# Kernel optimization log

Hardware: AMD Instinct MI355X
Metric: run time of the kernel (lower is better)

## Reference

```python
import jax, jax.numpy as jnp
import numpy as np

N, B, F, MAXDEG = 100000, 4096, 128, 128
NEI = [25, 10]          # FLAGS.num_neighbors = '25_10'
E1, E2 = 128, 64        # FLAGS.encoder = '128_64'
DEC, C = 256, 50        # FLAGS.decoder, num_classes


def setup_inputs() -> dict:
    key = jax.random.key(0)
    ks = jax.random.split(key, 12)
    return {
        'nodes': jax.random.randint(ks[0], (B,), 0, N),
        'adj_info': jax.random.randint(ks[1], (N, MAXDEG), 0, N),
        'degrees': jax.random.uniform(ks[2], (N,), minval=1.0, maxval=float(MAXDEG)),
        'features': jax.random.normal(ks[3], (N, F), dtype=jnp.float32),
        'W0': jax.random.normal(ks[4], (F, E1), dtype=jnp.float32) / np.sqrt(F),
        'Wm': jax.random.normal(ks[5], (E1, E2), dtype=jnp.float32) / np.sqrt(E1),
        'Ws': jax.random.normal(ks[6], (E1, E2), dtype=jnp.float32) / np.sqrt(E1),
        'W1': jax.random.normal(ks[7], (E2, DEC), dtype=jnp.float32) / np.sqrt(E2),
        'b1': jnp.zeros((DEC,), jnp.float32),
        'W2': jax.random.normal(ks[8], (DEC, C), dtype=jnp.float32) / np.sqrt(DEC),
        'b2': jnp.zeros((C,), jnp.float32),
    }


def _gc(self_v, neigh_v, neigh_d, W, act):
    # GraphSAGE-style degree-normalized mean aggregation + shared linear map
    neigh_mean = jnp.mean(neigh_v / neigh_d, axis=1)   # [n, d_in]
    return act((self_v + neigh_mean) @ W)


def reference(nodes, adj_info, degrees, features, W0, Wm, Ws, W1, b1, W2, b2):
    key = jax.random.key(42)
    k1, k2, k3 = jax.random.split(key, 3)
    # --- uniform neighbor sampling (shared column shuffle, as in TF code) ---
    # hop 1: t = L-1 -> NEI[1] = 10 samples per seed node
    p1 = jax.random.permutation(k1, MAXDEG)[: NEI[1]]
    nb1 = adj_info[nodes][:, p1].reshape(-1)            # [10*B]
    # hop 2: t = 0 -> NEI[0] = 25 samples per hop-1 node
    p2 = jax.random.permutation(k2, MAXDEG)[: NEI[0]]
    nb2 = adj_info[nb1][:, p2].reshape(-1)              # [250*B]

    samples = [nodes, nb1, nb2]
    deg = [degrees[s] for s in samples]
    x = [features[s] for s in samples]                  # [B,F],[10B,F],[250B,F]

    tanh = jnp.tanh
    # layer 0: convolve hops 0 and 1 with shared W0
    h0 = _gc(x[0], x[1].reshape(B, NEI[1], F), deg[1].reshape(B, NEI[1], 1), W0, tanh)
    h1 = _gc(x[1], x[2].reshape(NEI[1] * B, NEI[0], F), deg[2].reshape(NEI[1] * B, NEI[0], 1), W0, tanh)
    # layer 1 (last): mean / std heads, linear activation, hop 0 only
    ident = lambda t: t
    z_mean = _gc(h0, h1.reshape(B, NEI[1], E1), deg[1].reshape(B, NEI[1], 1), Wm, ident)
    z_std = _gc(h0, h1.reshape(B, NEI[1], E1), deg[1].reshape(B, NEI[1], 1), Ws, ident)
    # reparameterized sample (std head = log-std)
    eps = jax.random.normal(k3, z_mean.shape, dtype=z_mean.dtype)
    z = z_mean + eps * jnp.exp(z_std)
    # decoder MLP + softmax class prediction (S = 1 MC sample)
    logits = jax.nn.relu(z @ W1 + b1) @ W2 + b2
    return jax.nn.softmax(logits, axis=-1)
```

## Files before the change

kernel.cpp:

```cpp
#include <hip/hip_runtime.h>
#include <hip/hip_bf16.h>
#include <hip/hip_fp16.h>
#include <stdint.h>
#include <stddef.h>

#define NNODES  100000
#define BATCH   4096
#define FDIM    128
#define MAXDEG  128
#define NEI0    25
#define NEI1    10
#define E1D     128
#define E2D     64
#define DECD    256
#define NCLS    50

#define NH1     (BATCH * NEI1)
#define NROWS   (NH1 + BATCH)

typedef _Float16 half8 __attribute__((ext_vector_type(8)));
typedef float f32x4 __attribute__((ext_vector_type(4)));
typedef float f32x2 __attribute__((ext_vector_type(2)));

__host__ __device__ inline void tf2x32(uint32_t k0, uint32_t k1,
                                       uint32_t x0, uint32_t x1,
                                       uint32_t* o0, uint32_t* o1) {
  uint32_t ks[3] = {k0, k1, k0 ^ k1 ^ 0x1BD11BDAu};
  x0 += ks[0]; x1 += ks[1];
  const int rot[2][4] = {{13, 15, 26, 6}, {17, 29, 16, 24}};
  for (int i = 0; i < 5; ++i) {
    const int* r = rot[i & 1];
    for (int j = 0; j < 4; ++j) {
      x0 += x1;
      x1 = (x1 << r[j]) | (x1 >> (32 - r[j]));
      x1 ^= x0;
    }
    x0 += ks[(i + 1) % 3];
    x1 += ks[(i + 2) % 3] + (uint32_t)(i + 1);
  }
  *o0 = x0; *o1 = x1;
}

__device__ inline float erfinv_xla(float x) {
  float w = -log1pf(-x * x);
  float p;
  if (w < 5.0f) {
    w = w - 2.5f;
    p = 2.81022636e-08f;
    p = 3.43273939e-07f  + p * w;
    p = -3.5233877e-06f  + p * w;
    p = -4.39150654e-06f + p * w;
    p = 0.00021858087f   + p * w;
    p = -0.00125372503f  + p * w;
    p = -0.00417768164f  + p * w;
    p = 0.246640727f     + p * w;
    p = 1.50140941f      + p * w;
  } else {
    w = sqrtf(w) - 3.0f;
    p = -0.000200214257f;
    p = 0.000100950558f  + p * w;
    p = 0.00134934322f   + p * w;
    p = -0.00367342844f  + p * w;
    p = 0.00573950773f   + p * w;
    p = -0.0076224613f   + p * w;
    p = 0.00943887047f   + p * w;
    p = 1.00167406f      + p * w;
    p = 2.83297682f      + p * w;
  }
  return p * x;
}

struct PermArgs { int p1[NEI1]; int p2[NEI0]; };

#define CAST_FBLKS 12500
#define W0HT_BLKS  8
#define WMST_BLKS  8
#define W1T_BLKS   8
#define W2P_BLKS   8
#define NB1_BLKS   160

__global__ __launch_bounds__(256) void prep_kernel(const float* __restrict__ f,
                                                   uint8_t* __restrict__ fh8,
                                                   const float* __restrict__ W0,
                                                   __half* __restrict__ W0ht,
                                                   const float* __restrict__ Wm,
                                                   const float* __restrict__ Wsd,
                                                   __half* __restrict__ Wmst,
                                                   const float* __restrict__ W1,
                                                   __half* __restrict__ W1t,
                                                   const float* __restrict__ W2,
                                                   __half* __restrict__ W2p,
                                                   const int* __restrict__ nodes,
                                                   const int* __restrict__ adj,
                                                   const float* __restrict__ degrees,
                                                   int* __restrict__ nb1,
                                                   float* __restrict__ invd1, PermArgs pa) {
  int bx = blockIdx.x;
  if (bx < CAST_FBLKS) {
    int i = bx * 256 + threadIdx.x;
    float4 v = ((const float4*)f)[i];
    int p = 0;
    p = __builtin_amdgcn_cvt_pk_fp8_f32(v.x, v.y, p, false);
    p = __builtin_amdgcn_cvt_pk_fp8_f32(v.z, v.w, p, true);
    ((int*)fh8)[i] = p;
    return;
  }
  bx -= CAST_FBLKS;
  if (bx < W0HT_BLKS) {
    int i = bx * 256 + threadIdx.x;
    int n = i >> 4, kb = (i & 15) * 8;
    uint4 ov; uint32_t* op = (uint32_t*)&ov;
#pragma unroll
    for (int q = 0; q < 4; ++q) {
      __half2 h = __floats2half2_rn(W0[(size_t)(kb + 2 * q) * E1D + n],
                                    W0[(size_t)(kb + 2 * q + 1) * E1D + n]);
      op[q] = __builtin_bit_cast(uint32_t, h);
    }
    *(uint4*)(W0ht + (size_t)n * FDIM + kb) = ov;
    return;
  }
  bx -= W0HT_BLKS;
  if (bx < WMST_BLKS) {
    int i = bx * 256 + threadIdx.x;
    int n = i >> 4, kb = (i & 15) * 8;
    const float* src = (n < E2D) ? (Wm + n) : (Wsd + (n - E2D));
    uint4 ov; uint32_t* op = (uint32_t*)&ov;
#pragma unroll
    for (int q = 0; q < 4; ++q) {
      __half2 h = __floats2half2_rn(src[(size_t)(kb + 2 * q) * E2D],
                                    src[(size_t)(kb + 2 * q + 1) * E2D]);
      op[q] = __builtin_bit_cast(uint32_t, h);
    }
    *(uint4*)(Wmst + (size_t)n * E1D + kb) = ov;
    return;
  }
  bx -= WMST_BLKS;
  if (bx < W1T_BLKS) {
    int i = bx * 256 + threadIdx.x;
    int n = i >> 3, kb = (i & 7) * 8;
    uint4 ov; uint32_t* op = (uint32_t*)&ov;
#pragma unroll
    for (int q = 0; q < 4; ++q) {
      __half2 h = __floats2half2_rn(W1[(size_t)(kb + 2 * q) * DECD + n],
                                    W1[(size_t)(kb + 2 * q + 1) * DECD + n]);
      op[q] = __builtin_bit_cast(uint32_t, h);
    }
    *(uint4*)(W1t + (size_t)n * E2D + kb) = ov;
    return;
  }
  bx -= W1T_BLKS;
  if (bx < W2P_BLKS) {
    int i = bx * 256 + threadIdx.x;
    int c = i >> 5, kb = (i & 31) * 8;
    uint4 ov; uint32_t* op = (uint32_t*)&ov;
#pragma unroll
    for (int q = 0; q < 4; ++q) {
      float a = (c < NCLS) ? W2[(size_t)(kb + 2 * q) * NCLS + c] : 0.0f;
      float b = (c < NCLS) ? W2[(size_t)(kb + 2 * q + 1) * NCLS + c] : 0.0f;
      __half2 h = __floats2half2_rn(a, b);
      op[q] = __builtin_bit_cast(uint32_t, h);
    }
    *(uint4*)(W2p + (size_t)c * DECD + kb) = ov;
    return;
  }
  bx -= W2P_BLKS;
  {
    int i = bx * 256 + threadIdx.x;
    int b = i / NEI1, j = i - b * NEI1;
    int nn = adj[(size_t)nodes[b] * MAXDEG + pa.p1[j]];
    nb1[i] = nn;
    invd1[i] = 1.0f / degrees[nn];
  }
}

#define P2_BLKS   4000
#define SELF_BLKS 2816

__global__ __launch_bounds__(256) void prep2_kernel(const int* __restrict__ nodes,
                                                    const int* __restrict__ nb1,
                                                    const int* __restrict__ adj,
                                                    const float* __restrict__ degrees,
                                                    const float* __restrict__ features,
                                                    int* __restrict__ nb2,
                                                    float* __restrict__ invd2,
                                                    __half* __restrict__ selfh, PermArgs pa) {
  int bx = blockIdx.x;
  if (bx < P2_BLKS) {
    int i = bx * 256 + threadIdx.x;
    int r = i / NEI0, j = i - r * NEI0;
    int nn = adj[(size_t)nb1[r] * MAXDEG + pa.p2[j]];
    nb2[i] = nn;
    invd2[i] = 1.0f / degrees[nn];
    return;
  }
  {
    int i = (bx - P2_BLKS) * 256 + threadIdx.x;
    int row = i >> 4, cq = (i & 15) * 8;
    int nid = (row < NH1) ? nb1[row] : nodes[row - NH1];
    const float* src = features + (size_t)nid * FDIM + cq;
    float4 a = *(const float4*)src;
    float4 b = *(const float4*)(src + 4);
    uint4 ov; uint32_t* op = (uint32_t*)&ov;
    op[0] = __builtin_bit_cast(uint32_t, __floats2half2_rn(a.x, a.y));
    op[1] = __builtin_bit_cast(uint32_t, __floats2half2_rn(a.z, a.w));
    op[2] = __builtin_bit_cast(uint32_t, __floats2half2_rn(b.x, b.y));
    op[3] = __builtin_bit_cast(uint32_t, __floats2half2_rn(b.z, b.w));
    *(uint4*)(selfh + (size_t)row * FDIM + cq) = ov;
  }
}

#define CONSV8(vv, idv) do { \
    float id_ = (idv); \
    f32x2 c0_ = __builtin_amdgcn_cvt_pk_f32_fp8((int)(vv).x, false); \
    f32x2 c1_ = __builtin_amdgcn_cvt_pk_f32_fp8((int)(vv).x, true); \
    f32x2 c2_ = __builtin_amdgcn_cvt_pk_f32_fp8((int)(vv).y, false); \
    f32x2 c3_ = __builtin_amdgcn_cvt_pk_f32_fp8((int)(vv).y, true); \
    acc0 += c0_[0] * id_; acc1 += c0_[1] * id_; \
    acc2 += c1_[0] * id_; acc3 += c1_[1] * id_; \
    acc4 += c2_[0] * id_; acc5 += c2_[1] * id_; \
    acc6 += c3_[0] * id_; acc7 += c3_[1] * id_; \
  } while (0)

#define H8(x) __builtin_bit_cast(half8, x)

__global__ __launch_bounds__(256) void sage0_kernel(const int* __restrict__ nodes,
                                                    const int* __restrict__ nb1,
                                                    const float* __restrict__ invd1,
                                                    const int* __restrict__ nb2,
                                                    const float* __restrict__ invd2,
                                                    const uint8_t* __restrict__ fh8,
                                                    const __half* __restrict__ selfh,
                                                    const __half* __restrict__ W0ht,
                                                    __half* __restrict__ hh) {
  const int t = threadIdx.x;
  const int blk = blockIdx.x;
  const bool typeA = blk < (NH1 / 16);
  const int row_base = typeA ? blk * 16 : NH1 + (blk - NH1 / 16) * 16;
  __shared__ int    nn_lds[16][NEI0];
  __shared__ float  id_lds[16][NEI0];
  __shared__ __half agg_h[16][FDIM];

  if (typeA) {
    for (int i = t; i < 16 * NEI0; i += 256) {
      int r = i / NEI0, j = i - r * NEI0;
      nn_lds[r][j] = nb2[row_base * NEI0 + i];
      id_lds[r][j] = invd2[row_base * NEI0 + i];
    }
  } else {
    const int sb = row_base - NH1;
    if (t < 16 * NEI1) {
      int r = t / NEI1, j = t - r * NEI1;
      nn_lds[r][j] = nb1[sb * NEI1 + t];
      id_lds[r][j] = invd1[sb * NEI1 + t];
    }
  }
  __syncthreads();

  const int l = t & 63, w = t >> 6;
  const int r  = w * 4 + (l >> 4);
  const int c0 = (l & 15) * 8;
  const uint8_t* fr8 = fh8 + c0;
  const int*   nn_r = nn_lds[r];
  const float* id_r = id_lds[r];

  float acc0 = 0, acc1 = 0, acc2 = 0, acc3 = 0, acc4 = 0, acc5 = 0, acc6 = 0, acc7 = 0;
  uint4 gs = *(const uint4*)(selfh + (size_t)(row_base + r) * FDIM + c0);
  if (typeA) {
    uint2 g0  = *(const uint2*)(fr8 + (size_t)nn_r[0]  * FDIM);
    uint2 g1  = *(const uint2*)(fr8 + (size_t)nn_r[1]  * FDIM);
    uint2 g2  = *(const uint2*)(fr8 + (size_t)nn_r[2]  * FDIM);
    uint2 g3  = *(const uint2*)(fr8 + (size_t)nn_r[3]  * FDIM);
    uint2 g4  = *(const uint2*)(fr8 + (size_t)nn_r[4]  * FDIM);
    uint2 g5  = *(const uint2*)(fr8 + (size_t)nn_r[5]  * FDIM);
    uint2 g6  = *(const uint2*)(fr8 + (size_t)nn_r[6]  * FDIM);
    uint2 g7  = *(const uint2*)(fr8 + (size_t)nn_r[7]  * FDIM);
    uint2 g8  = *(const uint2*)(fr8 + (size_t)nn_r[8]  * FDIM);
    uint2 g9  = *(const uint2*)(fr8 + (size_t)nn_r[9]  * FDIM);
    uint2 g10 = *(const uint2*)(fr8 + (size_t)nn_r[10] * FDIM);
    uint2 g11 = *(const uint2*)(fr8 + (size_t)nn_r[11] * FDIM);
    uint2 g12 = *(const uint2*)(fr8 + (size_t)nn_r[12] * FDIM);
    uint2 g13 = *(const uint2*)(fr8 + (size_t)nn_r[13] * FDIM);
    uint2 g14 = *(const uint2*)(fr8 + (size_t)nn_r[14] * FDIM);
    uint2 g15 = *(const uint2*)(fr8 + (size_t)nn_r[15] * FDIM);
    uint2 g16 = *(const uint2*)(fr8 + (size_t)nn_r[16] * FDIM);
    uint2 g17 = *(const uint2*)(fr8 + (size_t)nn_r[17] * FDIM);
    uint2 g18 = *(const uint2*)(fr8 + (size_t)nn_r[18] * FDIM);
    uint2 g19 = *(const uint2*)(fr8 + (size_t)nn_r[19] * FDIM);
    uint2 g20 = *(const uint2*)(fr8 + (size_t)nn_r[20] * FDIM);
    uint2 g21 = *(const uint2*)(fr8 + (size_t)nn_r[21] * FDIM);
    uint2 g22 = *(const uint2*)(fr8 + (size_t)nn_r[22] * FDIM);
    uint2 g23 = *(const uint2*)(fr8 + (size_t)nn_r[23] * FDIM);
    uint2 g24 = *(const uint2*)(fr8 + (size_t)nn_r[24] * FDIM);
    __builtin_amdgcn_sched_barrier(0);
    CONSV8(g0,  id_r[0]);  CONSV8(g1,  id_r[1]);  CONSV8(g2,  id_r[2]);
    CONSV8(g3,  id_r[3]);  CONSV8(g4,  id_r[4]);  CONSV8(g5,  id_r[5]);
    CONSV8(g6,  id_r[6]);  CONSV8(g7,  id_r[7]);  CONSV8(g8,  id_r[8]);
    CONSV8(g9,  id_r[9]);  CONSV8(g10, id_r[10]); CONSV8(g11, id_r[11]);
    CONSV8(g12, id_r[12]); CONSV8(g13, id_r[13]); CONSV8(g14, id_r[14]);
    CONSV8(g15, id_r[15]); CONSV8(g16, id_r[16]); CONSV8(g17, id_r[17]);
    CONSV8(g18, id_r[18]); CONSV8(g19, id_r[19]); CONSV8(g20, id_r[20]);
    CONSV8(g21, id_r[21]); CONSV8(g22, id_r[22]); CONSV8(g23, id_r[23]);
    CONSV8(g24, id_r[24]);
  } else {
    uint2 g0 = *(const uint2*)(fr8 + (size_t)nn_r[0] * FDIM);
    uint2 g1 = *(const uint2*)(fr8 + (size_t)nn_r[1] * FDIM);
    uint2 g2 = *(const uint2*)(fr8 + (size_t)nn_r[2] * FDIM);
    uint2 g3 = *(const uint2*)(fr8 + (size_t)nn_r[3] * FDIM);
    uint2 g4 = *(const uint2*)(fr8 + (size_t)nn_r[4] * FDIM);
    uint2 g5 = *(const uint2*)(fr8 + (size_t)nn_r[5] * FDIM);
    uint2 g6 = *(const uint2*)(fr8 + (size_t)nn_r[6] * FDIM);
    uint2 g7 = *(const uint2*)(fr8 + (size_t)nn_r[7] * FDIM);
    uint2 g8 = *(const uint2*)(fr8 + (size_t)nn_r[8] * FDIM);
    uint2 g9 = *(const uint2*)(fr8 + (size_t)nn_r[9] * FDIM);
    __builtin_amdgcn_sched_barrier(0);
    CONSV8(g0, id_r[0]); CONSV8(g1, id_r[1]); CONSV8(g2, id_r[2]);
    CONSV8(g3, id_r[3]); CONSV8(g4, id_r[4]); CONSV8(g5, id_r[5]);
    CONSV8(g6, id_r[6]); CONSV8(g7, id_r[7]); CONSV8(g8, id_r[8]);
    CONSV8(g9, id_r[9]);
  }
  {
    const float sc = typeA ? (1.0f / NEI0) : (1.0f / NEI1);
    const __half2* sp = (const __half2*)&gs;
    float2 s0 = __half22float2(sp[0]);
    float2 s1 = __half22float2(sp[1]);
    float2 s2 = __half22float2(sp[2]);
    float2 s3 = __half22float2(sp[3]);
    uint4 ov; uint32_t* op = (uint32_t*)&ov;
    __half2 o0 = __floats2half2_rn(s0.x + acc0 * sc, s0.y + acc1 * sc);
    __half2 o1 = __floats2half2_rn(s1.x + acc2 * sc, s1.y + acc3 * sc);
    __half2 o2 = __floats2half2_rn(s2.x + acc4 * sc, s2.y + acc5 * sc);
    __half2 o3 = __floats2half2_rn(s3.x + acc6 * sc, s3.y + acc7 * sc);
    op[0] = __builtin_bit_cast(uint32_t, o0);
    op[1] = __builtin_bit_cast(uint32_t, o1);
    op[2] = __builtin_bit_cast(uint32_t, o2);
    op[3] = __builtin_bit_cast(uint32_t, o3);
    char* wb = (char*)agg_h + r * 256 + ((c0 * 2) ^ ((r & 7) << 4));
    *(uint4*)wb = ov;
  }
  __syncthreads();

  {
    const int lr = l & 15, kq = l >> 4;
    const __half* wt0 = W0ht + (size_t)(w * 32 + lr) * FDIM + kq * 8;
    const __half* wt1 = wt0 + 16 * FDIM;
    uint4 b00 = *(const uint4*)(wt0 + 0);
    uint4 b01 = *(const uint4*)(wt0 + 32);
    uint4 b02 = *(const uint4*)(wt0 + 64);
    uint4 b03 = *(const uint4*)(wt0 + 96);
    uint4 b10 = *(const uint4*)(wt1 + 0);
    uint4 b11 = *(const uint4*)(wt1 + 32);
    uint4 b12 = *(const uint4*)(wt1 + 64);
    uint4 b13 = *(const uint4*)(wt1 + 96);
    const char* ab = (const char*)agg_h + lr * 256;
    const int sw = (lr & 7) << 4;
    uint4 a0 = *(const uint4*)(ab + ((0 * 64 + kq * 16) ^ sw));
    uint4 a1 = *(const uint4*)(ab + ((1 * 64 + kq * 16) ^ sw));
    uint4 a2 = *(const uint4*)(ab + ((2 * 64 + kq * 16) ^ sw));
    uint4 a3 = *(const uint4*)(ab + ((3 * 64 + kq * 16) ^ sw));
    f32x4 cA = {0, 0, 0, 0}, cB = {0, 0, 0, 0};
    cA = __builtin_amdgcn_mfma_f32_16x16x32_f16(H8(a0), H8(b00), cA, 0, 0, 0);
    cB = __builtin_amdgcn_mfma_f32_16x16x32_f16(H8(a0), H8(b10), cB, 0, 0, 0);
    cA = __builtin_amdgcn_mfma_f32_16x16x32_f16(H8(a1), H8(b01), cA, 0, 0, 0);
    cB = __builtin_amdgcn_mfma_f32_16x16x32_f16(H8(a1), H8(b11), cB, 0, 0, 0);
    cA = __builtin_amdgcn_mfma_f32_16x16x32_f16(H8(a2), H8(b02), cA, 0, 0, 0);
    cB = __builtin_amdgcn_mfma_f32_16x16x32_f16(H8(a2), H8(b12), cB, 0, 0, 0);
    cA = __builtin_amdgcn_mfma_f32_16x16x32_f16(H8(a3), H8(b03), cA, 0, 0, 0);
    cB = __builtin_amdgcn_mfma_f32_16x16x32_f16(H8(a3), H8(b13), cB, 0, 0, 0);
    const int orow = row_base + (l >> 4) * 4;
    const int colA = w * 32 + lr, colB = colA + 16;
#pragma unroll
    for (int m = 0; m < 4; ++m) {
      hh[(size_t)(orow + m) * E1D + colA] = __float2half(tanhf(cA[m]));
      hh[(size_t)(orow + m) * E1D + colB] = __float2half(tanhf(cB[m]));
    }
  }
}

__global__ __launch_bounds__(256) void enc_kernel(const float* __restrict__ invd1,
                                                  const __half* __restrict__ hh,
                                                  const __half* __restrict__ Wmst,
                                                  __half* __restrict__ zh,
                                                  uint32_t k3a, uint32_t k3b) {
  const int t = threadIdx.x;
  const int s0 = blockIdx.x * 16;
  __shared__ float  id_lds[16][NEI1];
  __shared__ __half agg_h[16][FDIM];
  __shared__ float  P[16 * 132];

  if (t < 16 * NEI1) {
    int r = t / NEI1, j = t - r * NEI1;
    id_lds[r][j] = invd1[s0 * NEI1 + t];
  }
  __syncthreads();

  const int l = t & 63, w = t >> 6;
  const int r  = w * 4 + (l >> 4);
  const int c0 = (l & 15) * 8;

  float acc0 = 0, acc1 = 0, acc2 = 0, acc3 = 0, acc4 = 0, acc5 = 0, acc6 = 0, acc7 = 0;
  {
    const float* id_r = id_lds[r];
#pragma unroll
    for (int j = 0; j < NEI1; ++j) {
      uint4 vv = *(const uint4*)(hh + (size_t)((s0 + r) * NEI1 + j) * E1D + c0);
      const __half2* hp_ = (const __half2*)&vv;
      float id_ = id_r[j];
      float2 f0_ = __half22float2(hp_[0]);
      float2 f1_ = __half22float2(hp_[1]);
      float2 f2_ = __half22float2(hp_[2]);
      float2 f3_ = __half22float2(hp_[3]);
      acc0 += f0_.x * id_; acc1 += f0_.y * id_;
      acc2 += f1_.x * id_; acc3 += f1_.y * id_;
      acc4 += f2_.x * id_; acc5 += f2_.y * id_;
      acc6 += f3_.x * id_; acc7 += f3_.y * id_;
    }
    uint4 sv = *(const uint4*)(hh + (size_t)(NH1 + s0 + r) * E1D + c0);
    const float sc = 1.0f / NEI1;
    const __half2* sp = (const __half2*)&sv;
    float2 s0f = __half22float2(sp[0]);
    float2 s1f = __half22float2(sp[1]);
    float2 s2f = __half22float2(sp[2]);
    float2 s3f = __half22float2(sp[3]);
    uint4 ov; uint32_t* op = (uint32_t*)&ov;
    __half2 o0 = __floats2half2_rn(s0f.x + acc0 * sc, s0f.y + acc1 * sc);
    __half2 o1 = __floats2half2_rn(s1f.x + acc2 * sc, s1f.y + acc3 * sc);
    __half2 o2 = __floats2half2_rn(s2f.x + acc4 * sc, s2f.y + acc5 * sc);
    __half2 o3 = __floats2half2_rn(s3f.x + acc6 * sc, s3f.y + acc7 * sc);
    op[0] = __builtin_bit_cast(uint32_t, o0);
    op[1] = __builtin_bit_cast(uint32_t, o1);
    op[2] = __builtin_bit_cast(uint32_t, o2);
    op[3] = __builtin_bit_cast(uint32_t, o3);
    char* wb = (char*)agg_h + r * 256 + ((c0 * 2) ^ ((r & 7) << 4));
    *(uint4*)wb = ov;
  }
  __syncthreads();

  {
    const int lr = l & 15, kq = l >> 4;
    const __half* wt0 = Wmst + (size_t)(w * 32 + lr) * FDIM + kq * 8;
    const __half* wt1 = wt0 + 16 * FDIM;
    uint4 b00 = *(const uint4*)(wt0 + 0);
    uint4 b01 = *(const uint4*)(wt0 + 32);
    uint4 b02 = *(const uint4*)(wt0 + 64);
    uint4 b03 = *(const uint4*)(wt0 + 96);
    uint4 b10 = *(const uint4*)(wt1 + 0);
    uint4 b11 = *(const uint4*)(wt1 + 32);
    uint4 b12 = *(const uint4*)(wt1 + 64);
    uint4 b13 = *(const uint4*)(wt1 + 96);
    const char* ab = (const char*)agg_h + lr * 256;
    const int sw = (lr & 7) << 4;
    uint4 a0 = *(const uint4*)(ab + ((0 * 64 + kq * 16) ^ sw));
    uint4 a1 = *(const uint4*)(ab + ((1 * 64 + kq * 16) ^ sw));
    uint4 a2 = *(const uint4*)(ab + ((2 * 64 + kq * 16) ^ sw));
    uint4 a3 = *(const uint4*)(ab + ((3 * 64 + kq * 16) ^ sw));
    f32x4 cA = {0, 0, 0, 0}, cB = {0, 0, 0, 0};
    cA = __builtin_amdgcn_mfma_f32_16x16x32_f16(H8(a0), H8(b00), cA, 0, 0, 0);
    cB = __builtin_amdgcn_mfma_f32_16x16x32_f16(H8(a0), H8(b10), cB, 0, 0, 0);
    cA = __builtin_amdgcn_mfma_f32_16x16x32_f16(H8(a1), H8(b01), cA, 0, 0, 0);
    cB = __builtin_amdgcn_mfma_f32_16x16x32_f16(H8(a1), H8(b11), cB, 0, 0, 0);
    cA = __builtin_amdgcn_mfma_f32_16x16x32_f16(H8(a2), H8(b02), cA, 0, 0, 0);
    cB = __builtin_amdgcn_mfma_f32_16x16x32_f16(H8(a2), H8(b12), cB, 0, 0, 0);
    cA = __builtin_amdgcn_mfma_f32_16x16x32_f16(H8(a3), H8(b03), cA, 0, 0, 0);
    cB = __builtin_amdgcn_mfma_f32_16x16x32_f16(H8(a3), H8(b13), cB, 0, 0, 0);
    const int orow = kq * 4;
    const int colA = w * 32 + lr, colB = colA + 16;
#pragma unroll
    for (int m = 0; m < 4; ++m) {
      P[(orow + m) * 132 + colA] = cA[m];
      P[(orow + m) * 132 + colB] = cB[m];
    }
  }
  __syncthreads();

  {
    const int r2 = t >> 4;
    const int cb = (t & 15) * 4;
    uint32_t ph[2];
#pragma unroll
    for (int h = 0; h < 2; ++h) {
      float zv[2];
#pragma unroll
      for (int g = 0; g < 2; ++g) {
        int c = cb + 2 * h + g;
        uint32_t ctr = (uint32_t)((s0 + r2) * E2D + c);
        uint32_t y0, y1;
        tf2x32(k3a, k3b, 0u, ctr, &y0, &y1);
        uint32_t bits = y0 ^ y1;
        uint32_t fb = (bits >> 9) | 0x3F800000u;
        float fl = __uint_as_float(fb) - 1.0f;
        const float lo = -0.99999994f;
        float u = fmaxf(lo, fl * 2.0f + lo);
        float eps = 1.4142135381698608f * erfinv_xla(u);
        zv[g] = P[r2 * 132 + c] + eps * expf(P[r2 * 132 + c + E2D]);
      }
      ph[h] = __builtin_bit_cast(uint32_t, __floats2half2_rn(zv[0], zv[1]));
    }
    uint2 ov = make_uint2(ph[0], ph[1]);
    *(uint2*)(zh + (size_t)(s0 + r2) * E2D + cb) = ov;
  }
}

__global__ __launch_bounds__(256) void dec_kernel(const __half* __restrict__ zh,
                                                  const __half* __restrict__ W1t,
                                                  const float* __restrict__ b1,
                                                  const __half* __restrict__ W2p,
                                                  const float* __restrict__ b2,
                                                  float* __restrict__ out) {
  const int t = threadIdx.x;
  const int s0 = blockIdx.x * 16;
  __shared__ __half zA[16 * E2D];
  __shared__ float  hidF[16][260];
  __shared__ float  lgF[16][68];

  {
    int r = t >> 4, ch = (t & 15) * 4;
    uint2 v = *(const uint2*)(zh + (size_t)(s0 + r) * E2D + ch);
    char* p = (char*)zA + ((r * 128 + ch * 2) ^ ((r & 7) << 4));
    *(uint2*)p = v;
  }
  __syncthreads();

  const int l = t & 63, w = t >> 6;
  const int lr = l & 15, kq = l >> 4;

  {
    const char* zb = (const char*)zA + lr * 128;
    const int sw = (lr & 7) << 4;
    uint4 a0 = *(const uint4*)(zb + ((0 + kq * 16) ^ sw));
    uint4 a1 = *(const uint4*)(zb + ((64 + kq * 16) ^ sw));
#define G1STEP(CT) { \
    int n = w * 64 + (CT) * 16 + lr; \
    uint4 b0 = *(const uint4*)(W1t + (size_t)n * E2D + kq * 8); \
    uint4 b1v = *(const uint4*)(W1t + (size_t)n * E2D + 32 + kq * 8); \
    f32x4 cc = {0, 0, 0, 0}; \
    cc = __builtin_amdgcn_mfma_f32_16x16x32_f16(H8(a0), H8(b0), cc, 0, 0, 0); \
    cc = __builtin_amdgcn_mfma_f32_16x16x32_f16(H8(a1), H8(b1v), cc, 0, 0, 0); \
    float bv = b1[n]; \
    hidF[kq * 4 + 0][n] = fmaxf(cc[0] + bv, 0.0f); \
    hidF[kq * 4 + 1][n] = fmaxf(cc[1] + bv, 0.0f); \
    hidF[kq * 4 + 2][n] = fmaxf(cc[2] + bv, 0.0f); \
    hidF[kq * 4 + 3][n] = fmaxf(cc[3] + bv, 0.0f); }
    G1STEP(0) G1STEP(1) G1STEP(2) G1STEP(3)
#undef G1STEP
  }
  __syncthreads();

  {
    f32x4 d = {0, 0, 0, 0};
    const __half* w2b = W2p + (size_t)(w * 16 + lr) * DECD + kq * 8;
#pragma unroll
    for (int ks = 0; ks < 8; ++ks) {
      float4 fA = *(const float4*)&hidF[lr][ks * 32 + kq * 8];
      float4 fB = *(const float4*)&hidF[lr][ks * 32 + kq * 8 + 4];
      uint4 ap;
      uint32_t* app = (uint32_t*)&ap;
      app[0] = __builtin_bit_cast(uint32_t, __floats2half2_rn(fA.x, fA.y));
      app[1] = __builtin_bit_cast(uint32_t, __floats2half2_rn(fA.z, fA.w));
      app[2] = __builtin_bit_cast(uint32_t, __floats2half2_rn(fB.x, fB.y));
      app[3] = __builtin_bit_cast(uint32_t, __floats2half2_rn(fB.z, fB.w));
      uint4 bfr = *(const uint4*)(w2b + ks * 32);
      d = __builtin_amdgcn_mfma_f32_16x16x32_f16(H8(ap), H8(bfr), d, 0, 0, 0);
    }
    int col = w * 16 + lr;
    float bb = (col < NCLS) ? b2[col] : 0.0f;
#pragma unroll
    for (int m = 0; m < 4; ++m) lgF[kq * 4 + m][col] = d[m] + bb;
  }
  __syncthreads();

  {
#pragma unroll
    for (int rr = 0; rr < 4; ++rr) {
      int row = w * 4 + rr;
      float v = (l < NCLS) ? lgF[row][l] : -3.0e38f;
      float m = v;
#pragma unroll
      for (int off = 32; off; off >>= 1) m = fmaxf(m, __shfl_xor(m, off));
      float e = (l < NCLS) ? expf(v - m) : 0.0f;
      float s = e;
#pragma unroll
      for (int off = 32; off; off >>= 1) s += __shfl_xor(s, off);
      if (l < NCLS) out[(size_t)(s0 + row) * NCLS + l] = e / s;
    }
  }
}

static void host_permutation(uint32_t ka, uint32_t kb, int count, int* out_idx) {
  uint32_t sa, sb;
  tf2x32(ka, kb, 0u, 1u, &sa, &sb);
  uint32_t keys[MAXDEG];
  int vals[MAXDEG];
  for (int i = 0; i < MAXDEG; ++i) {
    uint32_t y0, y1;
    tf2x32(sa, sb, 0u, (uint32_t)i, &y0, &y1);
    keys[i] = y0 ^ y1;
    vals[i] = i;
  }
  for (int i = 1; i < MAXDEG; ++i) {
    uint32_t kk = keys[i]; int vv = vals[i]; int j = i - 1;
    while (j >= 0 && keys[j] > kk) { keys[j+1] = keys[j]; vals[j+1] = vals[j]; --j; }
    keys[j+1] = kk; vals[j+1] = vv;
  }
  for (int i = 0; i < count; ++i) out_idx[i] = vals[i];
}

extern "C" void kernel_launch(void* const* d_in, const int* in_sizes, int n_in,
                              void* d_out, int out_size, void* d_ws, size_t ws_size,
                              hipStream_t stream) {
  const int*   nodes    = (const int*)  d_in[0];
  const int*   adj      = (const int*)  d_in[1];
  const float* degrees  = (const float*)d_in[2];
  const float* features = (const float*)d_in[3];
  const float* W0       = (const float*)d_in[4];
  const float* Wm       = (const float*)d_in[5];
  const float* Wsd      = (const float*)d_in[6];
  const float* W1       = (const float*)d_in[7];
  const float* b1       = (const float*)d_in[8];
  const float* W2       = (const float*)d_in[9];
  const float* b2       = (const float*)d_in[10];
  float* out = (float*)d_out;

  uint32_t k1a, k1b, k2a, k2b, k3a, k3b;
  tf2x32(0u, 42u, 0u, 0u, &k1a, &k1b);
  tf2x32(0u, 42u, 0u, 1u, &k2a, &k2b);
  tf2x32(0u, 42u, 0u, 2u, &k3a, &k3b);

  PermArgs pa;
  host_permutation(k1a, k1b, NEI1, pa.p1);
  host_permutation(k2a, k2b, NEI0, pa.p2);

  char* ws = (char*)d_ws;
  int*     nb1   = (int*)    (ws + 0);
  float*   invd1 = (float*)  (ws + 163840);
  int*     nb2   = (int*)    (ws + 327680);
  float*   invd2 = (float*)  (ws + 4423680);
  __half*  hh    = (__half*) (ws + 8519680);
  __half*  zh    = (__half*) (ws + 20054016);
  uint8_t* fh8   = (uint8_t*)(ws + 20578304);
  __half*  selfh = (__half*) (ws + 33378304);
  __half*  W0ht  = (__half*) (ws + 44912640);
  __half*  Wmst  = (__half*) (ws + 44945408);
  __half*  W1t   = (__half*) (ws + 44978176);
  __half*  W2p   = (__half*) (ws + 45010944);

  prep_kernel<<<CAST_FBLKS + W0HT_BLKS + WMST_BLKS + W1T_BLKS + W2P_BLKS + NB1_BLKS,
                256, 0, stream>>>(
      features, fh8, W0, W0ht, Wm, Wsd, Wmst, W1, W1t, W2, W2p,
      nodes, adj, degrees, nb1, invd1, pa);
  prep2_kernel<<<P2_BLKS + SELF_BLKS, 256, 0, stream>>>(
      nodes, nb1, adj, degrees, features, nb2, invd2, selfh, pa);
  sage0_kernel<<<NROWS / 16, 256, 0, stream>>>(
      nodes, nb1, invd1, nb2, invd2, fh8, selfh, W0ht, hh);
  enc_kernel<<<BATCH / 16, 256, 0, stream>>>(invd1, hh, Wmst, zh, k3a, k3b);
  dec_kernel<<<BATCH / 16, 256, 0, stream>>>(zh, W1t, b1, W2p, b2, out);
}
```

Baseline: 72.79 us.

## Merge prep kernels by recomputing hop-1 ids and fuse encoder with decoder

Folds prep2 into prep_kernel. The hop-2 sampling and self-feature gather now recompute the hop-1 neighbor id from adj directly, so they no longer need the nb1 array written by an earlier launch. Also merges enc_kernel and dec_kernel: z is written into shared memory instead of a global buffer and the decoder MLP runs in the same block. This removes two launches, the kernel boundaries between them, and the z round trip through global memory, at the cost of redundant adjacency lookups and more shared memory per block.

Measured after the change: 68.01 us. -6.6%, faster.

```diff
diff --git a/kernel.cpp b/kernel.cpp
--- a/kernel.cpp
+++ b/kernel.cpp
@@ -72,12 +72,14 @@
 
 struct PermArgs { int p1[NEI1]; int p2[NEI0]; };
 
+#define NB1_BLKS   160
+#define P2_BLKS    4000
+#define SELF_BLKS  2816
 #define CAST_FBLKS 12500
 #define W0HT_BLKS  8
 #define WMST_BLKS  8
 #define W1T_BLKS   8
 #define W2P_BLKS   8
-#define NB1_BLKS   160
 
 __global__ __launch_bounds__(256) void prep_kernel(const float* __restrict__ f,
                                                    uint8_t* __restrict__ fh8,
@@ -94,8 +96,54 @@
                                                    const int* __restrict__ adj,
                                                    const float* __restrict__ degrees,
                                                    int* __restrict__ nb1,
-                                                   float* __restrict__ invd1, PermArgs pa) {
+                                                   float* __restrict__ invd1,
+                                                   int* __restrict__ nb2,
+                                                   float* __restrict__ invd2,
+                                                   __half* __restrict__ selfh,
+                                                   PermArgs pa) {
   int bx = blockIdx.x;
+  if (bx < NB1_BLKS) {
+    int i = bx * 256 + threadIdx.x;
+    int b = i / NEI1, j = i - b * NEI1;
+    int nn = adj[(size_t)nodes[b] * MAXDEG + pa.p1[j]];
+    nb1[i] = nn;
+    invd1[i] = 1.0f / degrees[nn];
+    return;
+  }
+  bx -= NB1_BLKS;
+  if (bx < P2_BLKS) {
+    int i = bx * 256 + threadIdx.x;
+    int r = i / NEI0, j = i - r * NEI0;
+    int b = r / NEI1, jj = r - b * NEI1;
+    int n1 = adj[(size_t)nodes[b] * MAXDEG + pa.p1[jj]];
+    int nn = adj[(size_t)n1 * MAXDEG + pa.p2[j]];
+    nb2[i] = nn;
+    invd2[i] = 1.0f / degrees[nn];
+    return;
+  }
+  bx -= P2_BLKS;
+  if (bx < SELF_BLKS) {
+    int i = bx * 256 + threadIdx.x;
+    int row = i >> 4, cq = (i & 15) * 8;
+    int nid;
+    if (row < NH1) {
+      int b = row / NEI1, jj = row - b * NEI1;
+      nid = adj[(size_t)nodes[b] * MAXDEG + pa.p1[jj]];
+    } else {
+      nid = nodes[row - NH1];
+    }
+    const float* src = f + (size_t)nid * FDIM + cq;
+    float4 a = *(const float4*)src;
+    float4 b4 = *(const float4*)(src + 4);
+    uint4 ov; uint32_t* op = (uint32_t*)&ov;
+    op[0] = __builtin_bit_cast(uint32_t, __floats2half2_rn(a.x, a.y));
+    op[1] = __builtin_bit_cast(uint32_t, __floats2half2_rn(a.z, a.w));
+    op[2] = __builtin_bit_cast(uint32_t, __floats2half2_rn(b4.x, b4.y));
+    op[3] = __builtin_bit_cast(uint32_t, __floats2half2_rn(b4.z, b4.w));
+    *(uint4*)(selfh + (size_t)row * FDIM + cq) = ov;
+    return;
+  }
+  bx -= SELF_BLKS;
   if (bx < CAST_FBLKS) {
     int i = bx * 256 + threadIdx.x;
     float4 v = ((const float4*)f)[i];
@@ -149,7 +197,7 @@
     return;
   }
   bx -= W1T_BLKS;
-  if (bx < W2P_BLKS) {
+  {
     int i = bx * 256 + threadIdx.x;
     int c = i >> 5, kb = (i & 31) * 8;
     uint4 ov; uint32_t* op = (uint32_t*)&ov;
@@ -161,51 +209,6 @@
       op[q] = __builtin_bit_cast(uint32_t, h);
     }
     *(uint4*)(W2p + (size_t)c * DECD + kb) = ov;
-    return;
-  }
-  bx -= W2P_BLKS;
-  {
-    int i = bx * 256 + threadIdx.x;
-    int b = i / NEI1, j = i - b * NEI1;
-    int nn = adj[(size_t)nodes[b] * MAXDEG + pa.p1[j]];
-    nb1[i] = nn;
-    invd1[i] = 1.0f / degrees[nn];
-  }
-}
-
-#define P2_BLKS   4000
-#define SELF_BLKS 2816
-
-__global__ __launch_bounds__(256) void prep2_kernel(const int* __restrict__ nodes,
-                                                    const int* __restrict__ nb1,
-                                                    const int* __restrict__ adj,
-                                                    const float* __restrict__ degrees,
-                                                    const float* __restrict__ features,
-                                                    int* __restrict__ nb2,
-                                                    float* __restrict__ invd2,
-                                                    __half* __restrict__ selfh, PermArgs pa) {
-  int bx = blockIdx.x;
-  if (bx < P2_BLKS) {
-    int i = bx * 256 + threadIdx.x;
-    int r = i / NEI0, j = i - r * NEI0;
-    int nn = adj[(size_t)nb1[r] * MAXDEG + pa.p2[j]];
-    nb2[i] = nn;
-    invd2[i] = 1.0f / degrees[nn];
-    return;
-  }
-  {
-    int i = (bx - P2_BLKS) * 256 + threadIdx.x;
-    int row = i >> 4, cq = (i & 15) * 8;
-    int nid = (row < NH1) ? nb1[row] : nodes[row - NH1];
-    const float* src = features + (size_t)nid * FDIM + cq;
-    float4 a = *(const float4*)src;
-    float4 b = *(const float4*)(src + 4);
-    uint4 ov; uint32_t* op = (uint32_t*)&ov;
-    op[0] = __builtin_bit_cast(uint32_t, __floats2half2_rn(a.x, a.y));
-    op[1] = __builtin_bit_cast(uint32_t, __floats2half2_rn(a.z, a.w));
-    op[2] = __builtin_bit_cast(uint32_t, __floats2half2_rn(b.x, b.y));
-    op[3] = __builtin_bit_cast(uint32_t, __floats2half2_rn(b.z, b.w));
-    *(uint4*)(selfh + (size_t)row * FDIM + cq) = ov;
   }
 }
 
@@ -376,16 +379,23 @@
   }
 }
 
-__global__ __launch_bounds__(256) void enc_kernel(const float* __restrict__ invd1,
-                                                  const __half* __restrict__ hh,
-                                                  const __half* __restrict__ Wmst,
-                                                  __half* __restrict__ zh,
-                                                  uint32_t k3a, uint32_t k3b) {
+__global__ __launch_bounds__(256) void encdec_kernel(const float* __restrict__ invd1,
+                                                     const __half* __restrict__ hh,
+                                                     const __half* __restrict__ Wmst,
+                                                     const __half* __restrict__ W1t,
+                                                     const float* __restrict__ b1,
+                                                     const __half* __restrict__ W2p,
+                                                     const float* __restrict__ b2,
+                                                     float* __restrict__ out,
+                                                     uint32_t k3a, uint32_t k3b) {
   const int t = threadIdx.x;
   const int s0 = blockIdx.x * 16;
   __shared__ float  id_lds[16][NEI1];
   __shared__ __half agg_h[16][FDIM];
   __shared__ float  P[16 * 132];
+  __shared__ __half zA[16 * E2D];
+  __shared__ float  hidF[16][260];
+  __shared__ float  lgF[16][68];
 
   if (t < 16 * NEI1) {
     int r = t / NEI1, j = t - r * NEI1;
@@ -394,11 +404,12 @@
   __syncthreads();
 
   const int l = t & 63, w = t >> 6;
-  const int r  = w * 4 + (l >> 4);
-  const int c0 = (l & 15) * 8;
-
-  float acc0 = 0, acc1 = 0, acc2 = 0, acc3 = 0, acc4 = 0, acc5 = 0, acc6 = 0, acc7 = 0;
-  {
+  const int lr = l & 15, kq = l >> 4;
+
+  {
+    const int r  = w * 4 + (l >> 4);
+    const int c0 = (l & 15) * 8;
+    float acc0 = 0, acc1 = 0, acc2 = 0, acc3 = 0, acc4 = 0, acc5 = 0, acc6 = 0, acc7 = 0;
     const float* id_r = id_lds[r];
 #pragma unroll
     for (int j = 0; j < NEI1; ++j) {
@@ -436,7 +447,6 @@
   __syncthreads();
 
   {
-    const int lr = l & 15, kq = l >> 4;
     const __half* wt0 = Wmst + (size_t)(w * 32 + lr) * FDIM + kq * 8;
     const __half* wt1 = wt0 + 16 * FDIM;
     uint4 b00 = *(const uint4*)(wt0 + 0);
@@ -495,33 +505,10 @@
       }
       ph[h] = __builtin_bit_cast(uint32_t, __floats2half2_rn(zv[0], zv[1]));
     }
-    uint2 ov = make_uint2(ph[0], ph[1]);
-    *(uint2*)(zh + (size_t)(s0 + r2) * E2D + cb) = ov;
-  }
-}
-
-__global__ __launch_bounds__(256) void dec_kernel(const __half* __restrict__ zh,
-                                                  const __half* __restrict__ W1t,
-                                                  const float* __restrict__ b1,
-                                                  const __half* __restrict__ W2p,
-                                                  const float* __restrict__ b2,
-                                                  float* __restrict__ out) {
-  const int t = threadIdx.x;
-  const int s0 = blockIdx.x * 16;
-  __shared__ __half zA[16 * E2D];
-  __shared__ float  hidF[16][260];
-  __shared__ float  lgF[16][68];
-
-  {
-    int r = t >> 4, ch = (t & 15) * 4;
-    uint2 v = *(const uint2*)(zh + (size_t)(s0 + r) * E2D + ch);
-    char* p = (char*)zA + ((r * 128 + ch * 2) ^ ((r & 7) << 4));
-    *(uint2*)p = v;
-  }
-  __syncthreads();
-
-  const int l = t & 63, w = t >> 6;
-  const int lr = l & 15, kq = l >> 4;
+    char* p = (char*)zA + ((r2 * 128 + cb * 2) ^ ((r2 & 7) << 4));
+    *(uint2*)p = make_uint2(ph[0], ph[1]);
+  }
+  __syncthreads();
 
   {
     const char* zb = (const char*)zA + lr * 128;
@@ -635,22 +622,19 @@
   int*     nb2   = (int*)    (ws + 327680);
   float*   invd2 = (float*)  (ws + 4423680);
   __half*  hh    = (__half*) (ws + 8519680);
-  __half*  zh    = (__half*) (ws + 20054016);
-  uint8_t* fh8   = (uint8_t*)(ws + 20578304);
-  __half*  selfh = (__half*) (ws + 33378304);
-  __half*  W0ht  = (__half*) (ws + 44912640);
-  __half*  Wmst  = (__half*) (ws + 44945408);
-  __half*  W1t   = (__half*) (ws + 44978176);
-  __half*  W2p   = (__half*) (ws + 45010944);
-
-  prep_kernel<<<CAST_FBLKS + W0HT_BLKS + WMST_BLKS + W1T_BLKS + W2P_BLKS + NB1_BLKS,
-                256, 0, stream>>>(
+  uint8_t* fh8   = (uint8_t*)(ws + 20054016);
+  __half*  selfh = (__half*) (ws + 32854016);
+  __half*  W0ht  = (__half*) (ws + 44388352);
+  __half*  Wmst  = (__half*) (ws + 44421120);
+  __half*  W1t   = (__half*) (ws + 44453888);
+  __half*  W2p   = (__half*) (ws + 44486656);
+
+  prep_kernel<<<NB1_BLKS + P2_BLKS + SELF_BLKS + CAST_FBLKS +
+                W0HT_BLKS + WMST_BLKS + W1T_BLKS + W2P_BLKS, 256, 0, stream>>>(
       features, fh8, W0, W0ht, Wm, Wsd, Wmst, W1, W1t, W2, W2p,
-      nodes, adj, degrees, nb1, invd1, pa);
-  prep2_kernel<<<P2_BLKS + SELF_BLKS, 256, 0, stream>>>(
-      nodes, nb1, adj, degrees, features, nb2, invd2, selfh, pa);
+      nodes, adj, degrees, nb1, invd1, nb2, invd2, selfh, pa);
   sage0_kernel<<<NROWS / 16, 256, 0, stream>>>(
       nodes, nb1, invd1, nb2, invd2, fh8, selfh, W0ht, hh);
-  enc_kernel<<<BATCH / 16, 256, 0, stream>>>(invd1, hh, Wmst, zh, k3a, k3b);
-  dec_kernel<<<BATCH / 16, 256, 0, stream>>>(zh, W1t, b1, W2p, b2, out);
+  encdec_kernel<<<BATCH / 16, 256, 0, stream>>>(
+      invd1, hh, Wmst, W1t, b1, W2p, b2, out, k3a, k3b);
 }
```
